# Performance work log

Measured on AMD Instinct MI355X. Metric: run time of the kernel, lower is better.

## Reference

```python
import jax, jax.numpy as jnp
import numpy as np

BATCH, NODES, FEAT, OUT, EIG = 32, 20000, 64, 64, 16

def setup_inputs() -> dict:
    key = jax.random.key(0)
    k1, k2, k3 = jax.random.split(key, 3)
    x = jax.random.normal(k1, (BATCH, NODES, FEAT), dtype=jnp.float32)
    V = jax.random.normal(k2, (NODES, EIG), dtype=jnp.float32)
    # G packs the ParameterList: G[j, i] == self.G[j*num_features + i]
    # (full EIG x EIG matrices; xavier_uniform_ overwrites the diag init)
    G = jax.random.normal(k3, (OUT, FEAT, EIG, EIG), dtype=jnp.float32) * 0.2
    return {"x": x, "V": V, "G": G}

def reference(x, V, G):
    # original: out[b, n, j] = sum_i (V @ G[j,i] @ V.T @ x[b,:,i]) [n]
    # z[b, i, f] = sum_m V[m, f] * x[b, m, i]        (project onto eigenbasis)
    z = jnp.einsum('mf,bmi->bif', V, x)
    # w[b, j, e] = sum_{i, f} G[j, i, e, f] * z[b, i, f]  (spectral filter mix)
    w = jnp.einsum('jief,bif->bje', G, z)
    # out[b, n, j] = sum_e V[n, e] * w[b, j, e]      (back to node space)
    out = jnp.einsum('ne,bje->bnj', V, w)
    return out
```

## Files before the change

### kernel.cpp

```cpp
#include <hip/hip_runtime.h>
#include <stdint.h>

#define BATCH 32
#define NODES 20000
#define FEAT  64
#define OUT   64
#define EIG   16

#define CH1      25
#define S1_NPB   800
#define S1_TILES 10
#define S1_TR    80

__device__ __forceinline__ void g2l16(const float* g, float* l) {
    __builtin_amdgcn_global_load_lds(
        (const __attribute__((address_space(1))) uint32_t*)(uintptr_t)g,
        (__attribute__((address_space(3))) uint32_t*)(uintptr_t)l,
        16, 0, 0);
}

#define FMA16(ii, xc) \
    acc[ii][0].x += (xc)*v0.x; acc[ii][0].y += (xc)*v0.y; acc[ii][0].z += (xc)*v0.z; acc[ii][0].w += (xc)*v0.w; \
    acc[ii][1].x += (xc)*v1.x; acc[ii][1].y += (xc)*v1.y; acc[ii][1].z += (xc)*v1.z; acc[ii][1].w += (xc)*v1.w; \
    acc[ii][2].x += (xc)*v2.x; acc[ii][2].y += (xc)*v2.y; acc[ii][2].z += (xc)*v2.z; acc[ii][2].w += (xc)*v2.w; \
    acc[ii][3].x += (xc)*v3.x; acc[ii][3].y += (xc)*v3.y; acc[ii][3].z += (xc)*v3.z; acc[ii][3].w += (xc)*v3.w;

__global__ __launch_bounds__(256)
void k_stage1(const float* __restrict__ x, const float* __restrict__ V,
              float* __restrict__ zpart) {
    const int c = blockIdx.x;
    const int b = blockIdx.y;
    const int t = threadIdx.x;
    const int lane = t & 63;
    const int wv   = t >> 6;
    const int ms   = lane >> 4;
    const int ig   = lane & 15;

    __shared__ __align__(16) float xs[2][S1_TR * FEAT];
    __shared__ __align__(16) float vs[2][S1_TR * EIG];

    const float* xg = x + ((size_t)b * NODES + (size_t)c * S1_NPB) * FEAT;
    const float* vg = V + (size_t)c * S1_NPB * EIG;

    auto stage = [&](int tt, int d) {
#pragma unroll
        for (int k = 0; k < 5; k++) {
            const int off = wv * 1280 + k * 256;
            g2l16(xg + (size_t)tt * S1_TR * FEAT + off + lane * 4, &xs[d][off]);
        }
#pragma unroll
        for (int k = 0; k < 2; k++) {
            const int callid = wv + k * 4;
            const int off = (callid > 4 ? 4 : callid) * 256;
            g2l16(vg + (size_t)tt * S1_TR * EIG + off + lane * 4, &vs[d][off]);
        }
    };

    float4 acc[4][4];
#pragma unroll
    for (int ii = 0; ii < 4; ii++)
#pragma unroll
        for (int q = 0; q < 4; q++) acc[ii][q] = make_float4(0.f,0.f,0.f,0.f);

    stage(0, 0);

    for (int tt = 0; tt < S1_TILES; tt++) {
        const int d = tt & 1;
        if (tt < S1_TILES - 1) {
            stage(tt + 1, d ^ 1);
            asm volatile("s_waitcnt vmcnt(7)" ::: "memory");
        } else {
            asm volatile("s_waitcnt vmcnt(0)" ::: "memory");
        }
        __builtin_amdgcn_s_barrier();
        __builtin_amdgcn_sched_barrier(0);

        const float* xt = &xs[d][wv * 20 * FEAT];
        const float* vt = &vs[d][wv * 20 * EIG];
#pragma unroll
        for (int itr = 0; itr < 5; itr++) {
            const int r = itr * 4 + ms;
            const float4 xv = *(const float4*)(xt + r * FEAT + ig * 4);
            const float4 v0 = *(const float4*)(vt + r * EIG);
            const float4 v1 = *(const float4*)(vt + r * EIG + 4);
            const float4 v2 = *(const float4*)(vt + r * EIG + 8);
            const float4 v3 = *(const float4*)(vt + r * EIG + 12);
            FMA16(0, xv.x); FMA16(1, xv.y); FMA16(2, xv.z); FMA16(3, xv.w);
        }
        __builtin_amdgcn_sched_barrier(0);
        __builtin_amdgcn_s_barrier();
    }

#pragma unroll
    for (int ii = 0; ii < 4; ii++)
#pragma unroll
        for (int q = 0; q < 4; q++) {
            acc[ii][q].x += __shfl_xor(acc[ii][q].x, 16); acc[ii][q].x += __shfl_xor(acc[ii][q].x, 32);
            acc[ii][q].y += __shfl_xor(acc[ii][q].y, 16); acc[ii][q].y += __shfl_xor(acc[ii][q].y, 32);
            acc[ii][q].z += __shfl_xor(acc[ii][q].z, 16); acc[ii][q].z += __shfl_xor(acc[ii][q].z, 32);
            acc[ii][q].w += __shfl_xor(acc[ii][q].w, 16); acc[ii][q].w += __shfl_xor(acc[ii][q].w, 32);
        }

    float4* zred = (float4*)&xs[0][0];
    __syncthreads();
    if (ms == 0) {
#pragma unroll
        for (int ii = 0; ii < 4; ii++)
#pragma unroll
            for (int q = 0; q < 4; q++)
                zred[wv * 256 + ig * 16 + ii * 4 + q] = acc[ii][q];
    }
    __syncthreads();

    float4 s  = zred[t];
    const float4 s1 = zred[256 + t];
    const float4 s2 = zred[512 + t];
    const float4 s3 = zred[768 + t];
    s.x += s1.x + s2.x + s3.x;
    s.y += s1.y + s2.y + s3.y;
    s.z += s1.z + s2.z + s3.z;
    s.w += s1.w + s2.w + s3.w;
    *(float4*)(zpart + ((size_t)c * BATCH + b) * (FEAT * EIG) + t * 4) = s;
}

__global__ void k_reduce(const float* __restrict__ zpart, float* __restrict__ z,
                         float* __restrict__ w) {
    const int b = blockIdx.y;
    const int t = threadIdx.x;
    if (blockIdx.x == 1) {
        ((float4*)w)[b * 256 + t] = make_float4(0.f, 0.f, 0.f, 0.f);
        return;
    }
    float4 s = make_float4(0.f, 0.f, 0.f, 0.f);
#pragma unroll
    for (int c = 0; c < CH1; c++) {
        const float4 v = ((const float4*)zpart)[((size_t)c * BATCH + b) * 256 + t];
        s.x += v.x; s.y += v.y; s.z += v.z; s.w += v.w;
    }
    ((float4*)z)[(size_t)b * 256 + t] = s;
}

__global__ void k_stage2(const float* __restrict__ G, const float* __restrict__ z,
                         float* __restrict__ w) {
    const int j  = blockIdx.x;
    const int iq = blockIdx.y;
    const int t = threadIdx.x;
    const int e  = t & 15;
    const int bh = t >> 4;

    __shared__ float zs[32][128];
#pragma unroll
    for (int r = 0; r < 4; r++) {
        const int g = t + 256 * r;
        const int bb = g >> 5, off = g & 31;
        ((float4*)&zs[bb][0])[off] =
            ((const float4*)z)[(size_t)bb * 256 + iq * 32 + off];
    }
    __syncthreads();

    const float* Gj = G + (size_t)j * FEAT * EIG * EIG;
    float acc0 = 0.f, acc1 = 0.f;

#pragma unroll 2
    for (int it = 0; it < 8; it++) {
        const int i = iq * 8 + it;
        const float4* gp = (const float4*)(Gj + ((size_t)i * EIG + e) * EIG);
        const float4 g0 = gp[0], g1 = gp[1], g2 = gp[2], g3 = gp[3];
        const float4* zA = (const float4*)&zs[bh][it * 16];
        const float4* zB = (const float4*)&zs[bh + 16][it * 16];
        const float4 a0 = zA[0], a1 = zA[1], a2 = zA[2], a3 = zA[3];
        const float4 b0 = zB[0], b1 = zB[1], b2 = zB[2], b3 = zB[3];
        acc0 += g0.x*a0.x + g0.y*a0.y + g0.z*a0.z + g0.w*a0.w
              + g1.x*a1.x + g1.y*a1.y + g1.z*a1.z + g1.w*a1.w
              + g2.x*a2.x + g2.y*a2.y + g2.z*a2.z + g2.w*a2.w
              + g3.x*a3.x + g3.y*a3.y + g3.z*a3.z + g3.w*a3.w;
        acc1 += g0.x*b0.x + g0.y*b0.y + g0.z*b0.z + g0.w*b0.w
              + g1.x*b1.x + g1.y*b1.y + g1.z*b1.z + g1.w*b1.w
              + g2.x*b2.x + g2.y*b2.y + g2.z*b2.z + g2.w*b2.w
              + g3.x*b3.x + g3.y*b3.y + g3.z*b3.z + g3.w*b3.w;
    }

    atomicAdd(&w[((size_t)bh * OUT + j) * EIG + e], acc0);
    atomicAdd(&w[((size_t)(bh + 16) * OUT + j) * EIG + e], acc1);
}

#define DOT16(u) (v0.x*W[u][0].x + v0.y*W[u][0].y + v0.z*W[u][0].z + v0.w*W[u][0].w \
                + v1.x*W[u][1].x + v1.y*W[u][1].y + v1.z*W[u][1].z + v1.w*W[u][1].w \
                + v2.x*W[u][2].x + v2.y*W[u][2].y + v2.z*W[u][2].z + v2.w*W[u][2].w \
                + v3.x*W[u][3].x + v3.y*W[u][3].y + v3.z*W[u][3].z + v3.w*W[u][3].w)

#define CH3 64

__global__ __launch_bounds__(128, 4)
void k_stage3(const float* __restrict__ V, const float* __restrict__ w,
              float* __restrict__ out) {
    const int c = blockIdx.x;
    const int b = blockIdx.y;
    const int t = threadIdx.x;
    const int jg = t & 15;
    const int ns = t >> 4;

    const float* wp = w + ((size_t)b * OUT + 4 * jg) * EIG;
    float4 W[4][4];
#pragma unroll
    for (int u = 0; u < 4; u++)
#pragma unroll
        for (int vr = 0; vr < 4; vr++)
            W[u][vr] = *(const float4*)(wp + u * EIG + vr * 4);

    const int nb = c * 320 + ns;
    float* ob = out + (size_t)b * NODES * OUT + 4 * jg;

    int n = nb;
    bool val = (n < NODES);
    float4 v0 = make_float4(0,0,0,0), v1 = v0, v2 = v0, v3 = v0;
    if (val) {
        const float* vp = V + (size_t)n * EIG;
        v0 = *(const float4*)(vp);      v1 = *(const float4*)(vp + 4);
        v2 = *(const float4*)(vp + 8);  v3 = *(const float4*)(vp + 12);
    }

    for (int it = 0; it < 40; it++) {
        const int n2 = nb + (it + 1) * 8;
        const bool val2 = (it < 39) && (n2 < NODES);
        float4 u0 = make_float4(0,0,0,0), u1 = u0, u2 = u0, u3 = u0;
        if (val2) {
            const float* vp = V + (size_t)n2 * EIG;
            u0 = *(const float4*)(vp);      u1 = *(const float4*)(vp + 4);
            u2 = *(const float4*)(vp + 8);  u3 = *(const float4*)(vp + 12);
        }
        if (val) {
            float4 o;
            o.x = DOT16(0); o.y = DOT16(1); o.z = DOT16(2); o.w = DOT16(3);
            *(float4*)(ob + (size_t)n * OUT) = o;
        }
        v0 = u0; v1 = u1; v2 = u2; v3 = u3;
        n = n2; val = val2;
    }
}

extern "C" void kernel_launch(void* const* d_in, const int* in_sizes, int n_in,
                              void* d_out, int out_size, void* d_ws, size_t ws_size,
                              hipStream_t stream) {
    const float* x = (const float*)d_in[0];
    const float* V = (const float*)d_in[1];
    const float* G = (const float*)d_in[2];
    float* out = (float*)d_out;

    float* z     = (float*)d_ws;
    float* w     = z + (size_t)BATCH * FEAT * EIG;
    float* zpart = w + (size_t)BATCH * OUT * EIG;

    k_stage1<<<dim3(CH1, BATCH), 256, 0, stream>>>(x, V, zpart);
    k_reduce<<<dim3(2, BATCH), 256, 0, stream>>>(zpart, z, w);
    k_stage2<<<dim3(OUT, 8), 256, 0, stream>>>(G, z, w);
    k_stage3<<<dim3(CH3, BATCH), 128, 0, stream>>>(V, w, out);
}
```

Before: 323.6 us.

## Use per-wave LDS staging in stage1 and widen stage3 blocks with nontemporal stores

Stage1 now gives each wave its own LDS slices and loads only the rows it consumes, so the two block-wide barriers per tile are removed. The V tile tail is loaded with a 4-byte global-to-LDS load. Stage3 moves to 256-thread blocks covering 16 rows per iteration, remaps block indices to swizzle chunk order, and writes output with nontemporal stores to avoid polluting cache. The risk is the per-wave vmcnt accounting: the tile now issues 7 loads per wave with a waitcnt of 7, and a wrong count would read stale LDS.

```diff
diff --git a/kernel.cpp b/kernel.cpp
--- a/kernel.cpp
+++ b/kernel.cpp
@@ -10,7 +10,6 @@
 #define CH1      25
 #define S1_NPB   800
 #define S1_TILES 10
-#define S1_TR    80
 
 __device__ __forceinline__ void g2l16(const float* g, float* l) {
     __builtin_amdgcn_global_load_lds(
@@ -18,6 +17,12 @@
         (__attribute__((address_space(3))) uint32_t*)(uintptr_t)l,
         16, 0, 0);
 }
+__device__ __forceinline__ void g2l4(const float* g, float* l) {
+    __builtin_amdgcn_global_load_lds(
+        (const __attribute__((address_space(1))) uint32_t*)(uintptr_t)g,
+        (__attribute__((address_space(3))) uint32_t*)(uintptr_t)l,
+        4, 0, 0);
+}
 
 #define FMA16(ii, xc) \
     acc[ii][0].x += (xc)*v0.x; acc[ii][0].y += (xc)*v0.y; acc[ii][0].z += (xc)*v0.z; acc[ii][0].w += (xc)*v0.w; \
@@ -36,24 +41,20 @@
     const int ms   = lane >> 4;
     const int ig   = lane & 15;
 
-    __shared__ __align__(16) float xs[2][S1_TR * FEAT];
-    __shared__ __align__(16) float vs[2][S1_TR * EIG];
-
-    const float* xg = x + ((size_t)b * NODES + (size_t)c * S1_NPB) * FEAT;
-    const float* vg = V + (size_t)c * S1_NPB * EIG;
+    __shared__ __align__(16) float xsl[2][4][20 * FEAT];
+    __shared__ __align__(16) float vsl[2][4][20 * EIG];
+
+    const float* xw = x + ((size_t)b * NODES + (size_t)c * S1_NPB + wv * 20) * FEAT;
+    const float* vw = V + ((size_t)c * S1_NPB + wv * 20) * EIG;
 
     auto stage = [&](int tt, int d) {
-#pragma unroll
-        for (int k = 0; k < 5; k++) {
-            const int off = wv * 1280 + k * 256;
-            g2l16(xg + (size_t)tt * S1_TR * FEAT + off + lane * 4, &xs[d][off]);
-        }
-#pragma unroll
-        for (int k = 0; k < 2; k++) {
-            const int callid = wv + k * 4;
-            const int off = (callid > 4 ? 4 : callid) * 256;
-            g2l16(vg + (size_t)tt * S1_TR * EIG + off + lane * 4, &vs[d][off]);
-        }
+        const float* xsrc = xw + (size_t)tt * 80 * FEAT;
+        const float* vsrc = vw + (size_t)tt * 80 * EIG;
+#pragma unroll
+        for (int k = 0; k < 5; k++)
+            g2l16(xsrc + k * 256 + lane * 4, &xsl[d][wv][k * 256]);
+        g2l16(vsrc + lane * 4, &vsl[d][wv][0]);
+        g2l4 (vsrc + 256 + lane, &vsl[d][wv][256]);
     };
 
     float4 acc[4][4];
@@ -72,11 +73,10 @@
         } else {
             asm volatile("s_waitcnt vmcnt(0)" ::: "memory");
         }
-        __builtin_amdgcn_s_barrier();
         __builtin_amdgcn_sched_barrier(0);
 
-        const float* xt = &xs[d][wv * 20 * FEAT];
-        const float* vt = &vs[d][wv * 20 * EIG];
+        const float* xt = &xsl[d][wv][0];
+        const float* vt = &vsl[d][wv][0];
 #pragma unroll
         for (int itr = 0; itr < 5; itr++) {
             const int r = itr * 4 + ms;
@@ -87,8 +87,6 @@
             const float4 v3 = *(const float4*)(vt + r * EIG + 12);
             FMA16(0, xv.x); FMA16(1, xv.y); FMA16(2, xv.z); FMA16(3, xv.w);
         }
-        __builtin_amdgcn_sched_barrier(0);
-        __builtin_amdgcn_s_barrier();
     }
 
 #pragma unroll
@@ -101,7 +99,7 @@
             acc[ii][q].w += __shfl_xor(acc[ii][q].w, 16); acc[ii][q].w += __shfl_xor(acc[ii][q].w, 32);
         }
 
-    float4* zred = (float4*)&xs[0][0];
+    float4* zred = (float4*)&xsl[0][0][0];
     __syncthreads();
     if (ms == 0) {
 #pragma unroll
@@ -191,10 +189,13 @@
 
 #define CH3 64
 
-__global__ __launch_bounds__(128, 4)
+typedef float f32x4 __attribute__((ext_vector_type(4)));
+
+__global__ __launch_bounds__(256)
 void k_stage3(const float* __restrict__ V, const float* __restrict__ w,
               float* __restrict__ out) {
-    const int c = blockIdx.x;
+    const int craw = blockIdx.x;
+    const int c = (craw & 7) * 8 + (craw >> 3);
     const int b = blockIdx.y;
     const int t = threadIdx.x;
     const int jg = t & 15;
@@ -220,9 +221,9 @@
         v2 = *(const float4*)(vp + 8);  v3 = *(const float4*)(vp + 12);
     }
 
-    for (int it = 0; it < 40; it++) {
-        const int n2 = nb + (it + 1) * 8;
-        const bool val2 = (it < 39) && (n2 < NODES);
+    for (int it = 0; it < 20; it++) {
+        const int n2 = nb + (it + 1) * 16;
+        const bool val2 = (it < 19) && (n2 < NODES);
         float4 u0 = make_float4(0,0,0,0), u1 = u0, u2 = u0, u3 = u0;
         if (val2) {
             const float* vp = V + (size_t)n2 * EIG;
@@ -230,9 +231,9 @@
             u2 = *(const float4*)(vp + 8);  u3 = *(const float4*)(vp + 12);
         }
         if (val) {
-            float4 o;
-            o.x = DOT16(0); o.y = DOT16(1); o.z = DOT16(2); o.w = DOT16(3);
-            *(float4*)(ob + (size_t)n * OUT) = o;
+            f32x4 o;
+            o[0] = DOT16(0); o[1] = DOT16(1); o[2] = DOT16(2); o[3] = DOT16(3);
+            __builtin_nontemporal_store(o, (f32x4*)(ob + (size_t)n * OUT));
         }
         v0 = u0; v1 = u1; v2 = u2; v3 = u3;
         n = n2; val = val2;
@@ -254,5 +255,5 @@
     k_stage1<<<dim3(CH1, BATCH), 256, 0, stream>>>(x, V, zpart);
     k_reduce<<<dim3(2, BATCH), 256, 0, stream>>>(zpart, z, w);
     k_stage2<<<dim3(OUT, 8), 256, 0, stream>>>(G, z, w);
-    k_stage3<<<dim3(CH3, BATCH), 128, 0, stream>>>(V, w, out);
-}
+    k_stage3<<<dim3(CH3, BATCH), 256, 0, stream>>>(V, w, out);
+}
```

Measured after the change: 318.7 us. No clear change (-1.5%).
